# Optimization experiments

Measured on AMD Instinct MI355X. Metric: run time of the kernel, lower is better.

Reference implementation:

```python
import jax, jax.numpy as jnp
import numpy as np


def setup_inputs() -> dict:
    key = jax.random.key(0)
    k1, k2 = jax.random.split(key)
    B, V = 256, 128000
    logits = jax.random.normal(k1, (B, V), dtype=jnp.float32)
    temperatures = jax.random.uniform(k2, (B,), dtype=jnp.float32, minval=0.0, maxval=1.5)
    # make a quarter of the sequences greedy (temperature == 0) to exercise both paths
    temperatures = temperatures.at[: B // 4].set(0.0)
    return {"logits": logits, "temperatures": temperatures}


def reference(logits, temperatures):
    # Temperature-scaled logits; temperature==0 rows use temp 1 for the (unused) sampling path.
    logits = logits.astype(jnp.float32)
    safe_t = jnp.where(temperatures == 0, jnp.ones_like(temperatures), temperatures)
    scaled = logits / safe_t[:, None]  # [B, V]

    # probs (same math as torch.softmax(scaled, -1)); materialized for faithfulness
    probs = jax.nn.softmax(scaled, axis=-1)

    greedy_tokens = jnp.argmax(logits, axis=-1)  # [B]

    # torch.multinomial(probs, 1) == Gumbel-max / categorical over scaled logits
    sample_key = jax.random.key(42)
    sampled_tokens = jax.random.categorical(sample_key, scaled, axis=-1)  # [B]

    return jnp.where(temperatures == 0, greedy_tokens, sampled_tokens)
```

## Files before the change

### kernel.cpp

```cpp
#include <hip/hip_runtime.h>
#include <stdint.h>

namespace {

constexpr int kB = 256;
constexpr int kV = 128000;
constexpr int kSplit = 25;
constexpr int kBlk = 256;
constexpr int kChunk = kV / kSplit;
constexpr int kIter = kChunk / (kBlk * 4);

struct Part { float val; int idx; };

__device__ __forceinline__ uint32_t threefry_bits(uint32_t x1) {
  constexpr uint32_t ks0 = 0u;
  constexpr uint32_t ks1 = 42u;
  constexpr uint32_t ks2 = 0x1BD11BDAu ^ ks0 ^ ks1;
  uint32_t x0 = ks0;
  x1 += ks1;
#define TF_ROUND(r) { x0 += x1; x1 = __builtin_rotateleft32(x1, r); x1 ^= x0; }
  TF_ROUND(13) TF_ROUND(15) TF_ROUND(26) TF_ROUND(6)
  x0 += ks1; x1 += ks2 + 1u;
  TF_ROUND(17) TF_ROUND(29) TF_ROUND(16) TF_ROUND(24)
  x0 += ks2; x1 += ks0 + 2u;
  TF_ROUND(13) TF_ROUND(15) TF_ROUND(26) TF_ROUND(6)
  x0 += ks0; x1 += ks1 + 3u;
  TF_ROUND(17) TF_ROUND(29) TF_ROUND(16) TF_ROUND(24)
  x0 += ks1; x1 += ks2 + 4u;
  TF_ROUND(13) TF_ROUND(15) TF_ROUND(26) TF_ROUND(6)
  x0 += ks2; x1 += ks0 + 5u;
#undef TF_ROUND
  return x0 ^ x1;
}

__device__ __forceinline__ float gumbel_from_bits(uint32_t bits) {
  constexpr float kTiny = 1.17549435e-38f;
  constexpr float kNegLn2 = -0.69314718055994530942f;
  float f = __uint_as_float((bits >> 9) | 0x3F800000u) - 1.0f;
  float u = f + kTiny;
  float y = __builtin_amdgcn_logf(u) * kNegLn2;
  return __builtin_amdgcn_logf(y) * kNegLn2;
}

__global__ __launch_bounds__(kBlk) void sampler_partial(
    const float* __restrict__ logits, const float* __restrict__ temps,
    Part* __restrict__ parts) {
  const int r = blockIdx.x / kSplit;
  const int g = blockIdx.x % kSplit;
  const float t = temps[r];
  const int start = g * kChunk;
  const float* __restrict__ row = logits + (size_t)r * kV;
  const int tbase = start + (int)threadIdx.x * 4;

  float4 a[kIter];
#pragma unroll
  for (int it = 0; it < kIter; ++it) {
    a[it] = *reinterpret_cast<const float4*>(row + tbase + it * kBlk * 4);
  }

  float best = -__builtin_inff();
  int bi = 0;

  if (t == 0.0f) {
#pragma unroll
    for (int it = 0; it < kIter; ++it) {
      const int v = tbase + it * kBlk * 4;
      float la[4] = {a[it].x, a[it].y, a[it].z, a[it].w};
#pragma unroll
      for (int j = 0; j < 4; ++j) {
        if (la[j] > best) { best = la[j]; bi = v + j; }
      }
    }
  } else {
#pragma unroll
    for (int it = 0; it < kIter; ++it) {
      const int v = tbase + it * kBlk * 4;
      const uint32_t base = (uint32_t)(r * kV + v);
      float la[4] = {a[it].x, a[it].y, a[it].z, a[it].w};
#pragma unroll
      for (int j = 0; j < 4; ++j) {
        float gb = gumbel_from_bits(threefry_bits(base + (uint32_t)j));
        float key = fmaf(t, gb, la[j]);
        if (key > best) { best = key; bi = v + j; }
      }
    }
  }

  __shared__ float sv[kBlk];
  __shared__ int si[kBlk];
  sv[threadIdx.x] = best;
  si[threadIdx.x] = bi;
  __syncthreads();
  for (int s = kBlk / 2; s > 0; s >>= 1) {
    if ((int)threadIdx.x < s) {
      float ov = sv[threadIdx.x + s]; int oi = si[threadIdx.x + s];
      float mv = sv[threadIdx.x];     int mi = si[threadIdx.x];
      if (ov > mv || (ov == mv && oi < mi)) {
        sv[threadIdx.x] = ov; si[threadIdx.x] = oi;
      }
    }
    __syncthreads();
  }
  if (threadIdx.x == 0) {
    parts[r * kSplit + g].val = sv[0];
    parts[r * kSplit + g].idx = si[0];
  }
}

__global__ __launch_bounds__(kB) void sampler_final(
    const Part* __restrict__ parts, int* __restrict__ out) {
  const int r = threadIdx.x;
  if (r < kB) {
    float bv = -__builtin_inff();
    int bi = 0;
#pragma unroll
    for (int g = 0; g < kSplit; ++g) {
      Part p = parts[r * kSplit + g];
      if (p.val > bv || (p.val == bv && p.idx < bi)) { bv = p.val; bi = p.idx; }
    }
    out[r] = bi;
  }
}

}

extern "C" void kernel_launch(void* const* d_in, const int* in_sizes, int n_in,
                              void* d_out, int out_size, void* d_ws, size_t ws_size,
                              hipStream_t stream) {
  const float* logits = (const float*)d_in[0];
  const float* temps = (const float*)d_in[1];
  int* out = (int*)d_out;
  Part* parts = (Part*)d_ws;

  sampler_partial<<<dim3(kB * kSplit), dim3(kBlk), 0, stream>>>(logits, temps, parts);
  sampler_final<<<dim3(1), dim3(kB), 0, stream>>>(parts, out);
}
```

Measured before the change: 208.9 us.

## Process five chunks per block with double-buffered register prefetch

Each block now handles five contiguous chunks of a row instead of one, and the next chunk's float4 loads are issued before the current chunk is processed, using a two-slot register buffer. This cuts the grid from 6400 to 1280 blocks, amortizes the shared-memory reduction, and overlaps memory loads with the threefry/Gumbel compute. In exchange register pressure doubles (two buffers of kIter float4), which may lower occupancy, and fewer blocks give less latency hiding across waves.

```diff
diff --git a/kernel.cpp b/kernel.cpp
--- a/kernel.cpp
+++ b/kernel.cpp
@@ -5,10 +5,12 @@
 
 constexpr int kB = 256;
 constexpr int kV = 128000;
+constexpr int kBlk = 256;
 constexpr int kSplit = 25;
-constexpr int kBlk = 256;
 constexpr int kChunk = kV / kSplit;
 constexpr int kIter = kChunk / (kBlk * 4);
+constexpr int kChunksPerBlk = 5;
+constexpr int kSubs = kSplit / kChunksPerBlk;
 
 struct Part { float val; int idx; };
 
@@ -45,56 +47,74 @@
 __global__ __launch_bounds__(kBlk) void sampler_partial(
     const float* __restrict__ logits, const float* __restrict__ temps,
     Part* __restrict__ parts) {
-  const int r = blockIdx.x / kSplit;
-  const int g = blockIdx.x % kSplit;
+  const int r = blockIdx.x / kSubs;
+  const int s = blockIdx.x % kSubs;
   const float t = temps[r];
-  const int start = g * kChunk;
   const float* __restrict__ row = logits + (size_t)r * kV;
-  const int tbase = start + (int)threadIdx.x * 4;
+  const int tid4 = (int)threadIdx.x * 4;
 
-  float4 a[kIter];
-#pragma unroll
-  for (int it = 0; it < kIter; ++it) {
-    a[it] = *reinterpret_cast<const float4*>(row + tbase + it * kBlk * 4);
+  float4 buf[2][kIter];
+
+#define LOAD_CHUNK(k, p)                                                     \
+  {                                                                          \
+    const int cs_ = (s * kChunksPerBlk + (k)) * kChunk + tid4;               \
+    _Pragma("unroll")                                                        \
+    for (int i_ = 0; i_ < kIter; ++i_)                                       \
+      buf[p][i_] = *reinterpret_cast<const float4*>(row + cs_ + i_ * kBlk * 4); \
   }
 
   float best = -__builtin_inff();
   int bi = 0;
 
+  LOAD_CHUNK(0, 0)
+
   if (t == 0.0f) {
 #pragma unroll
-    for (int it = 0; it < kIter; ++it) {
-      const int v = tbase + it * kBlk * 4;
-      float la[4] = {a[it].x, a[it].y, a[it].z, a[it].w};
+    for (int k = 0; k < kChunksPerBlk; ++k) {
+      if (k + 1 < kChunksPerBlk) LOAD_CHUNK(k + 1, (k + 1) & 1)
+      const int cs = (s * kChunksPerBlk + k) * kChunk + tid4;
 #pragma unroll
-      for (int j = 0; j < 4; ++j) {
-        if (la[j] > best) { best = la[j]; bi = v + j; }
+      for (int i = 0; i < kIter; ++i) {
+        const int v = cs + i * kBlk * 4;
+        float la[4] = {buf[k & 1][i].x, buf[k & 1][i].y,
+                       buf[k & 1][i].z, buf[k & 1][i].w};
+#pragma unroll
+        for (int j = 0; j < 4; ++j) {
+          if (la[j] > best) { best = la[j]; bi = v + j; }
+        }
       }
     }
   } else {
 #pragma unroll
-    for (int it = 0; it < kIter; ++it) {
-      const int v = tbase + it * kBlk * 4;
-      const uint32_t base = (uint32_t)(r * kV + v);
-      float la[4] = {a[it].x, a[it].y, a[it].z, a[it].w};
+    for (int k = 0; k < kChunksPerBlk; ++k) {
+      if (k + 1 < kChunksPerBlk) LOAD_CHUNK(k + 1, (k + 1) & 1)
+      const int cs = (s * kChunksPerBlk + k) * kChunk + tid4;
 #pragma unroll
-      for (int j = 0; j < 4; ++j) {
-        float gb = gumbel_from_bits(threefry_bits(base + (uint32_t)j));
-        float key = fmaf(t, gb, la[j]);
-        if (key > best) { best = key; bi = v + j; }
+      for (int i = 0; i < kIter; ++i) {
+        const int v = cs + i * kBlk * 4;
+        const uint32_t base = (uint32_t)(r * kV + v);
+        float la[4] = {buf[k & 1][i].x, buf[k & 1][i].y,
+                       buf[k & 1][i].z, buf[k & 1][i].w};
+#pragma unroll
+        for (int j = 0; j < 4; ++j) {
+          float gb = gumbel_from_bits(threefry_bits(base + (uint32_t)j));
+          float key = fmaf(t, gb, la[j]);
+          if (key > best) { best = key; bi = v + j; }
+        }
       }
     }
   }
+#undef LOAD_CHUNK
 
   __shared__ float sv[kBlk];
   __shared__ int si[kBlk];
   sv[threadIdx.x] = best;
   si[threadIdx.x] = bi;
   __syncthreads();
-  for (int s = kBlk / 2; s > 0; s >>= 1) {
-    if ((int)threadIdx.x < s) {
-      float ov = sv[threadIdx.x + s]; int oi = si[threadIdx.x + s];
-      float mv = sv[threadIdx.x];     int mi = si[threadIdx.x];
+  for (int st = kBlk / 2; st > 0; st >>= 1) {
+    if ((int)threadIdx.x < st) {
+      float ov = sv[threadIdx.x + st]; int oi = si[threadIdx.x + st];
+      float mv = sv[threadIdx.x];      int mi = si[threadIdx.x];
       if (ov > mv || (ov == mv && oi < mi)) {
         sv[threadIdx.x] = ov; si[threadIdx.x] = oi;
       }
@@ -102,8 +122,8 @@
     __syncthreads();
   }
   if (threadIdx.x == 0) {
-    parts[r * kSplit + g].val = sv[0];
-    parts[r * kSplit + g].idx = si[0];
+    parts[r * kSubs + s].val = sv[0];
+    parts[r * kSubs + s].idx = si[0];
   }
 }
 
@@ -114,8 +134,8 @@
     float bv = -__builtin_inff();
     int bi = 0;
 #pragma unroll
-    for (int g = 0; g < kSplit; ++g) {
-      Part p = parts[r * kSplit + g];
+    for (int g = 0; g < kSubs; ++g) {
+      Part p = parts[r * kSubs + g];
       if (p.val > bv || (p.val == bv && p.idx < bi)) { bv = p.val; bi = p.idx; }
     }
     out[r] = bi;
@@ -132,6 +152,6 @@
   int* out = (int*)d_out;
   Part* parts = (Part*)d_ws;
 
-  sampler_partial<<<dim3(kB * kSplit), dim3(kBlk), 0, stream>>>(logits, temps, parts);
+  sampler_partial<<<dim3(kB * kSubs), dim3(kBlk), 0, stream>>>(logits, temps, parts);
   sampler_final<<<dim3(1), dim3(kB), 0, stream>>>(parts, out);
 }
```

After: 204.9 us. About the same (-1.9%).
